# Kernel optimization log

Measured on AMD Instinct MI355X. Metric: run time of the kernel, lower is better.

The kernel has to match this reference:

```python
import jax, jax.numpy as jnp
import numpy as np

# Config (mirrors init_kwargs)
B, S = 1, 2048          # batch, seq_len
H = 2048                # hidden_size
NH, NKV = 16, 8         # attention heads, kv heads (GQA n_rep = 2)
HD = H // NH            # head_dim = 128
I = 5632                # intermediate_size
L = 2                   # num_hidden_layers
V = 32000               # vocab_size
WIN = 1024              # sliding_window
THETA = 10000.0
EPS = 1e-6


def setup_inputs() -> dict:
    key = jax.random.key(0)
    ks = jax.random.split(key, 12)
    s = 0.02
    return {
        "input_ids": jax.random.randint(ks[0], (B, S), 0, V, dtype=jnp.int32),
        "embed": jax.random.normal(ks[1], (V, H), jnp.float32) * s,
        "Wq": jax.random.normal(ks[2], (L, H, NH * HD), jnp.float32) * s,
        "Wk": jax.random.normal(ks[3], (L, H, NKV * HD), jnp.float32) * s,
        "Wv": jax.random.normal(ks[4], (L, H, NKV * HD), jnp.float32) * s,
        "Wo": jax.random.normal(ks[5], (L, NH * HD, H), jnp.float32) * s,
        "Wg": jax.random.normal(ks[6], (L, H, I), jnp.float32) * s,
        "Wu": jax.random.normal(ks[7], (L, H, I), jnp.float32) * s,
        "Wd": jax.random.normal(ks[8], (L, I, H), jnp.float32) * s,
        "ln1": jnp.ones((L, H), jnp.float32),
        "ln2": jnp.ones((L, H), jnp.float32),
        "norm_w": jnp.ones((H,), jnp.float32),
    }


def _rmsnorm(x, w, eps=EPS):
    return x * jax.lax.rsqrt(jnp.mean(x * x, axis=-1, keepdims=True) + eps) * w


def _rope_tables(seq_len, dim, theta):
    inv_freq = 1.0 / (theta ** (jnp.arange(0, dim, 2, dtype=jnp.float32) / dim))
    freqs = jnp.arange(seq_len, dtype=jnp.float32)[:, None] * inv_freq[None, :]  # [S, dim/2]
    emb = jnp.concatenate([freqs, freqs], axis=-1)  # [S, dim]
    return jnp.cos(emb), jnp.sin(emb)


def _rotate_half(x):
    half = x.shape[-1] // 2
    return jnp.concatenate([-x[..., half:], x[..., :half]], axis=-1)


def _sliding_window_causal_mask(seq_len, window, dtype):
    i = jnp.arange(seq_len)[:, None]
    j = jnp.arange(seq_len)[None, :]
    allowed = (j <= i) & (j >= i - window)  # band: causal + sliding window
    return jnp.where(allowed, 0.0, jnp.finfo(dtype).min).astype(dtype)[None, None]  # [1,1,S,S]


def _forward(input_ids, embed, Wq, Wk, Wv, Wo, Wg, Wu, Wd, ln1, ln2, norm_w):
    x = embed[input_ids]  # [B,S,H]
    cos, sin = _rope_tables(S, HD, THETA)          # [S,HD]
    cos = cos[None, :, None, :]                    # [1,S,1,HD]
    sin = sin[None, :, None, :]
    mask = _sliding_window_causal_mask(S, WIN, x.dtype)  # [1,1,S,S]
    scale = 1.0 / jnp.sqrt(jnp.float32(HD)).astype(x.dtype)
    n_rep = NH // NKV

    for l in range(L):
        # --- attention block ---
        h = _rmsnorm(x, ln1[l])
        q = (h @ Wq[l]).reshape(B, S, NH, HD)
        k = (h @ Wk[l]).reshape(B, S, NKV, HD)
        v = (h @ Wv[l]).reshape(B, S, NKV, HD)
        q = q * cos + _rotate_half(q) * sin
        k = k * cos + _rotate_half(k) * sin
        # repeat_kv (GQA)
        k = jnp.broadcast_to(k[:, :, :, None, :], (B, S, NKV, n_rep, HD)).reshape(B, S, NH, HD)
        v = jnp.broadcast_to(v[:, :, :, None, :], (B, S, NKV, n_rep, HD)).reshape(B, S, NH, HD)
        scores = jnp.einsum('bshn,bthn->bhst', q, k) * scale + mask  # [B,NH,S,S]
        attn = jax.nn.softmax(scores.astype(jnp.float32), axis=-1).astype(x.dtype)
        o = jnp.einsum('bhst,bthn->bshn', attn, v).reshape(B, S, NH * HD)
        x = x + o @ Wo[l]
        # --- MLP block (SwiGLU) ---
        h = _rmsnorm(x, ln2[l])
        x = x + (jax.nn.silu(h @ Wg[l]) * (h @ Wu[l])) @ Wd[l]

    return _rmsnorm(x, norm_w)


def reference(input_ids, embed, Wq, Wk, Wv, Wo, Wg, Wu, Wd, ln1, ln2, norm_w):
    return _forward(input_ids, embed, Wq, Wk, Wv, Wo, Wg, Wu, Wd, ln1, ln2, norm_w)
```

## Files before the change

### kernel.cpp

```cpp
#include <hip/hip_runtime.h>
#include <stdint.h>

using bf16x8 = __attribute__((ext_vector_type(8))) __bf16;
using f32x4  = __attribute__((ext_vector_type(4))) float;

#define DEVI __device__ __forceinline__

DEVI unsigned short f2b(float f) {
  unsigned int u = __builtin_bit_cast(unsigned int, f);
  u = (u + 0x7FFFu + ((u >> 16) & 1u)) >> 16;
  return (unsigned short)u;
}
DEVI float b2f(unsigned short h) {
  unsigned int u = ((unsigned int)h) << 16;
  return __builtin_bit_cast(float, u);
}
DEVI f32x4 mfma16(bf16x8 a, bf16x8 b, f32x4 c) {
  return __builtin_amdgcn_mfma_f32_16x16x32_bf16(a, b, c, 0, 0, 0);
}
#define GLD(gp, lp) __builtin_amdgcn_global_load_lds( \
    (__attribute__((address_space(1))) void*)(uintptr_t)(gp), \
    (__attribute__((address_space(3))) void*)(uintptr_t)(lp), 16, 0, 0)

static constexpr int S_LEN = 2048;
static constexpr int HDIM  = 2048;
static constexpr int NH    = 16;
static constexpr int NKV   = 8;
static constexpr int HD    = 128;
static constexpr int IFF   = 5632;
static constexpr int WIN   = 1024;

DEVI void rms_finish(float4 v0, float4 v1, const float* __restrict__ w,
                     void* __restrict__ outp, int s, int t, int outf32) {
  float ss = v0.x*v0.x + v0.y*v0.y + v0.z*v0.z + v0.w*v0.w +
             v1.x*v1.x + v1.y*v1.y + v1.z*v1.z + v1.w*v1.w;
  #pragma unroll
  for (int off = 32; off >= 1; off >>= 1) ss += __shfl_xor(ss, off, 64);
  __shared__ float red[4];
  if ((t & 63) == 0) red[t >> 6] = ss;
  __syncthreads();
  ss = red[0] + red[1] + red[2] + red[3];
  float rr = rsqrtf(ss * (1.0f / 2048.0f) + 1e-6f);
  const float4* w4 = (const float4*)w;
  float4 w0 = w4[t], w1 = w4[t + 256];
  float o0x = v0.x*rr*w0.x, o0y = v0.y*rr*w0.y, o0z = v0.z*rr*w0.z, o0w = v0.w*rr*w0.w;
  float o1x = v1.x*rr*w1.x, o1y = v1.y*rr*w1.y, o1z = v1.z*rr*w1.z, o1w = v1.w*rr*w1.w;
  if (outf32) {
    float4* o4 = (float4*)outp + (size_t)s * 512;
    o4[t]       = make_float4(o0x, o0y, o0z, o0w);
    o4[t + 256] = make_float4(o1x, o1y, o1z, o1w);
  } else {
    uint2* ob = (uint2*)((unsigned short*)outp + (size_t)s * HDIM);
    ob[t]       = make_uint2((unsigned)f2b(o0x) | ((unsigned)f2b(o0y) << 16),
                             (unsigned)f2b(o0z) | ((unsigned)f2b(o0w) << 16));
    ob[t + 256] = make_uint2((unsigned)f2b(o1x) | ((unsigned)f2b(o1y) << 16),
                             (unsigned)f2b(o1z) | ((unsigned)f2b(o1w) << 16));
  }
}

__global__ __launch_bounds__(256) void gather_kernel(const int* __restrict__ ids,
    const float* __restrict__ embed, float* __restrict__ x,
    float* __restrict__ ct, float* __restrict__ st,
    const float* __restrict__ ln1w, unsigned short* __restrict__ h) {
  int s = blockIdx.x, t = threadIdx.x;
  const float4* src = (const float4*)(embed + (size_t)ids[s] * HDIM);
  float4* dst = (float4*)(x + (size_t)s * HDIM);
  float4 v0 = src[t], v1 = src[t + 256];
  dst[t]       = v0;
  dst[t + 256] = v1;
  if (t < 64) {
    float inv = expf(-(float)t * (9.210340371976184f / 64.0f));
    float f = (float)s * inv;
    ct[s * 64 + t] = cosf(f);
    st[s * 64 + t] = sinf(f);
  }
  rms_finish(v0, v1, ln1w, h, s, t, 0);
}

template<int OUTF32, int NPARTS>
__global__ __launch_bounds__(256) void rmsnorm_combine_kernel(
    float* __restrict__ x, const unsigned short* __restrict__ parts,
    const float* __restrict__ w, void* __restrict__ outp) {
  int s = blockIdx.x, t = threadIdx.x;
  const size_t PS = (size_t)2048 * 2048;
  float4* row = (float4*)(x + (size_t)s * HDIM);
  float4 v0 = row[t], v1 = row[t + 256];
  #pragma unroll
  for (int p = 0; p < NPARTS; ++p) {
    const unsigned short* pr = parts + p * PS + (size_t)s * HDIM;
    uint2 a = *(const uint2*)(pr + t * 4);
    uint2 b = *(const uint2*)(pr + (t + 256) * 4);
    v0.x += b2f((unsigned short)a.x); v0.y += b2f((unsigned short)(a.x >> 16));
    v0.z += b2f((unsigned short)a.y); v0.w += b2f((unsigned short)(a.y >> 16));
    v1.x += b2f((unsigned short)b.x); v1.y += b2f((unsigned short)(b.x >> 16));
    v1.z += b2f((unsigned short)b.y); v1.w += b2f((unsigned short)(b.y >> 16));
  }
  row[t] = v0; row[t + 256] = v1;
  rms_finish(v0, v1, w, outp, s, t, OUTF32);
}

__global__ __launch_bounds__(256) void convert_weights_kernel(
    const float* __restrict__ Wq, const float* __restrict__ Wk,
    const float* __restrict__ Wv, const float* __restrict__ Wo,
    const float* __restrict__ Wg, const float* __restrict__ Wu,
    const float* __restrict__ Wd,
    unsigned short* wqkvT, unsigned short* woT,
    unsigned short* wguT, unsigned short* wdT) {
  __shared__ float tl[128 * 65];
  int b = blockIdx.x;
  const float* in; unsigned short* out; int istr, ostr, tilesN, t; int guAdd = -1;
  if (b < 512)       { in = Wq; out = wqkvT;                       istr = 2048; ostr = 2048; tilesN = 32; t = b; }
  else if (b < 768)  { in = Wk; out = wqkvT + (size_t)2048 * 2048; istr = 1024; ostr = 2048; tilesN = 16; t = b - 512; }
  else if (b < 1024) { in = Wv; out = wqkvT + (size_t)3072 * 2048; istr = 1024; ostr = 2048; tilesN = 16; t = b - 768; }
  else if (b < 1536) { in = Wo; out = woT;                         istr = 2048; ostr = 2048; tilesN = 32; t = b - 1024; }
  else if (b < 2944) { in = Wg; out = wguT;                        istr = 5632; ostr = 2048; tilesN = 88; t = b - 1536; guAdd = 0; }
  else if (b < 4352) { in = Wu; out = wguT;                        istr = 5632; ostr = 2048; tilesN = 88; t = b - 2944; guAdd = 128; }
  else               { in = Wd; out = wdT;                         istr = 2048; ostr = 5632; tilesN = 32; t = b - 4352; }
  int k0 = (t / tilesN) * 128, n0 = (t % tilesN) * 64;
  int tx = threadIdx.x & 63, ty = threadIdx.x >> 6;
  #pragma unroll
  for (int i = 0; i < 32; ++i)
    tl[(ty + 4 * i) * 65 + tx] = in[(size_t)(k0 + ty + 4 * i) * istr + (n0 + tx)];
  __syncthreads();
  int ob = (guAdd >= 0) ? (((n0 >> 7) << 8) + (n0 & 64) + guAdd) : n0;
  unsigned int* ou = (unsigned int*)out;
  const int kstr2 = ostr >> 1;
  #pragma unroll
  for (int i = 0; i < 16; ++i) {
    int nrow = ty + 4 * i;
    float lo = tl[(2 * tx) * 65 + nrow], hi = tl[(2 * tx + 1) * 65 + nrow];
    ou[(size_t)(ob + nrow) * kstr2 + (k0 >> 1) + tx] =
        (unsigned int)f2b(lo) | ((unsigned int)f2b(hi) << 16);
  }
}

DEVI bf16x8 ldsAB(const unsigned short* buf, int r, int cbyte) {
  return *(const bf16x8*)((const unsigned char*)buf + r * 128 + (cbyte ^ ((r & 7) << 4)));
}
DEVI void stage_unit(const unsigned short* __restrict__ G, int Kstr,
                     unsigned short* lbuf, int loff0, int grow0,
                     int loff1, int grow1, int w, int l) {
  const int rsub = l >> 3;
  const int ce = ((l & 7) ^ rsub) << 3;
  const unsigned short* s0 = G + (size_t)(grow0 + w * 8 + rsub) * Kstr + ce;
  GLD(s0, (unsigned char*)lbuf + loff0 + w * 1024 + l * 16);
  const unsigned short* s1 = G + (size_t)(grow1 + w * 8 + rsub) * Kstr + ce;
  GLD(s1, (unsigned char*)lbuf + loff1 + w * 1024 + l * 16);
}
template<int Q>
DEVI void phase128(const unsigned short* Ab, f32x4 (&acc)[4][4],
                   bf16x8 (&breg)[2][4], int wr, int lg, int li) {
  const int r0 = wr * 64 + Q * 16 + li;
  bf16x8 a0 = ldsAB(Ab, r0, lg * 16);
  bf16x8 a1 = ldsAB(Ab, r0, 64 + lg * 16);
  __builtin_amdgcn_s_setprio(1);
  #pragma unroll
  for (int n = 0; n < 4; ++n) acc[Q][n] = mfma16(a0, breg[0][n], acc[Q][n]);
  #pragma unroll
  for (int n = 0; n < 4; ++n) acc[Q][n] = mfma16(a1, breg[1][n], acc[Q][n]);
  __builtin_amdgcn_s_setprio(0);
}

template<int EPI>
__global__ __launch_bounds__(512, 1) void gemm128_kernel(
    const unsigned short* __restrict__ A, const unsigned short* __restrict__ Bt,
    void* __restrict__ Cout, int Kstr, int nt, int parts, int nbm, int ldc,
    long long partStride,
    const float* __restrict__ ct, const float* __restrict__ st,
    unsigned short* __restrict__ ko, unsigned short* __restrict__ vt) {
  __shared__ __align__(16) unsigned char smem[131072];
  unsigned short* As0 = (unsigned short*)smem;
  unsigned short* Bs0 = (unsigned short*)(smem + 32768);
  const int tid = threadIdx.x, l = tid & 63, w = tid >> 6;
  const int lg = l >> 4, li = l & 15;
  const int wr = w >> 2, wc = w & 3;
  const int nb = gridDim.x, qx = nb >> 3;
  const int wg = ((int)blockIdx.x & 7) * qx + ((int)blockIdx.x >> 3);
  const int nbT = nb / parts;
  const int tile = wg % nbT, part = wg / nbT;
  const int m0 = (tile % nbm) * 128, n0 = (tile / nbm) * 256;
  const int kOff = part * (nt << 6);
  const unsigned short* At  = A  + (size_t)m0 * Kstr + kOff;
  const unsigned short* Bto = Bt + (size_t)n0 * Kstr + kOff;
  f32x4 acc[4][4] = {};
  bf16x8 breg[2][4];

  stage_unit(Bto, Kstr, Bs0, 0, 0, 8192, 64, w, l);
  stage_unit(Bto, Kstr, Bs0, 16384, 128, 24576, 192, w, l);
  stage_unit(At,  Kstr, As0, 0, 0, 8192, 64, w, l);
  { int k1 = (nt > 1) ? 64 : 0;
    stage_unit(Bto + k1, Kstr, Bs0 + 16384, 0, 0, 8192, 64, w, l);
    stage_unit(Bto + k1, Kstr, Bs0 + 16384, 16384, 128, 24576, 192, w, l); }
  asm volatile("s_waitcnt vmcnt(4)\n\ts_barrier" ::: "memory");

  for (int t = 0; t < nt; ++t) {
    unsigned short* Ab  = As0 + (t & 1) * 8192;
    unsigned short* Bb  = Bs0 + (t & 1) * 16384;
    unsigned short* Abn = As0 + ((t & 1) ^ 1) * 8192;
    const int kt1 = ((t + 1 < nt) ? t + 1 : nt - 1) << 6;
    const int kt2 = ((t + 2 < nt) ? t + 2 : nt - 1) << 6;
    stage_unit(At + kt1, Kstr, Abn, 0, 0, 8192, 64, w, l);
    #pragma unroll
    for (int ks = 0; ks < 2; ++ks)
      #pragma unroll
      for (int n = 0; n < 4; ++n)
        breg[ks][n] = ldsAB(Bb, wc * 64 + n * 16 + li, ks * 64 + lg * 16);
    asm volatile("s_waitcnt lgkmcnt(0)\n\ts_barrier" ::: "memory");
    phase128<0>(Ab, acc, breg, wr, lg, li);
    stage_unit(Bto + kt2, Kstr, Bb, 0, 0, 8192, 64, w, l);
    phase128<1>(Ab, acc, breg, wr, lg, li);
    stage_unit(Bto + kt2, Kstr, Bb, 16384, 128, 24576, 192, w, l);
    phase128<2>(Ab, acc, breg, wr, lg, li);
    phase128<3>(Ab, acc, breg, wr, lg, li);
    asm volatile("s_waitcnt vmcnt(4) lgkmcnt(0)\n\ts_barrier" ::: "memory");
  }
  asm volatile("s_waitcnt vmcnt(0)" ::: "memory");

  if (EPI == 0) {
    unsigned short* C = (unsigned short*)Cout + (size_t)part * (size_t)partStride;
    #pragma unroll
    for (int m = 0; m < 4; ++m)
      #pragma unroll
      for (int n = 0; n < 4; ++n) {
        int col = n0 + wc * 64 + n * 16 + li;
        #pragma unroll
        for (int r = 0; r < 4; ++r) {
          int row = m0 + wr * 64 + m * 16 + lg * 4 + r;
          C[(size_t)row * ldc + col] = f2b(acc[m][n][r]);
        }
      }
  } else if (EPI == 3) {
    float* ub = (float*)smem;
    asm volatile("s_barrier" ::: "memory");
    if (wc >= 2) {
      #pragma unroll
      for (int m = 0; m < 4; ++m)
        #pragma unroll
        for (int n = 0; n < 4; ++n) {
          int colL = (wc - 2) * 64 + n * 16 + li;
          #pragma unroll
          for (int r = 0; r < 4; ++r) {
            int rowl = wr * 64 + m * 16 + lg * 4 + r;
            ub[rowl * 128 + colL] = acc[m][n][r];
          }
        }
    }
    asm volatile("s_waitcnt lgkmcnt(0)\n\ts_barrier" ::: "memory");
    if (wc < 2) {
      unsigned short* act = (unsigned short*)Cout;
      const int col0 = n0 >> 1;
      #pragma unroll
      for (int m = 0; m < 4; ++m)
        #pragma unroll
        for (int n = 0; n < 4; ++n) {
          int colL = wc * 64 + n * 16 + li;
          #pragma unroll
          for (int r = 0; r < 4; ++r) {
            int rowl = wr * 64 + m * 16 + lg * 4 + r;
            float g = acc[m][n][r];
            float u = ub[rowl * 128 + colL];
            act[(size_t)(m0 + rowl) * ldc + col0 + colL] =
                f2b(g / (1.0f + __expf(-g)) * u);
          }
        }
    }
  } else {
    float* dump = (float*)smem;
    asm volatile("s_barrier" ::: "memory");
    #pragma unroll
    for (int m = 0; m < 4; ++m)
      #pragma unroll
      for (int n = 0; n < 4; ++n) {
        int colL = wc * 64 + n * 16 + li;
        #pragma unroll
        for (int r = 0; r < 4; ++r) {
          int rowl = wr * 64 + m * 16 + lg * 4 + r;
          dump[rowl * 256 + colL] = acc[m][n][r];
        }
      }
    asm volatile("s_waitcnt lgkmcnt(0)\n\ts_barrier" ::: "memory");
    if (n0 < 3072) {
      unsigned short* qk = (n0 < 2048) ? (unsigned short*)Cout : ko;
      const int cbase = (n0 < 2048) ? n0 : (n0 - 2048);
      const int ostr  = (n0 < 2048) ? 2048 : 1024;
      #pragma unroll
      for (int m = 0; m < 4; ++m)
        #pragma unroll
        for (int n = 0; n < 4; ++n) {
          int colL = wc * 64 + n * 16 + li;
          int hi = colL & 64;
          #pragma unroll
          for (int r = 0; r < 4; ++r) {
            int rowl = wr * 64 + m * 16 + lg * 4 + r;
            int s = m0 + rowl;
            float own = dump[rowl * 256 + colL];
            float par = dump[rowl * 256 + (colL ^ 64)];
            float c  = ct[s * 64 + (colL & 63)];
            float sn = st[s * 64 + (colL & 63)];
            float v = hi ? (own * c + par * sn) : (own * c - par * sn);
            qk[(size_t)s * ostr + cbase + colL] = f2b(v);
          }
        }
    } else {
      int vcol = tid >> 1, sh = (tid & 1) * 64;
      unsigned short* dstp = vt + (size_t)(n0 - 3072 + vcol) * 2048 + m0 + sh;
      #pragma unroll
      for (int c8 = 0; c8 < 8; ++c8) {
        unsigned short pk[8];
        #pragma unroll
        for (int i = 0; i < 8; ++i)
          pk[i] = f2b(dump[(sh + c8 * 8 + i) * 256 + vcol]);
        *(uint4*)(dstp + c8 * 8) = *(const uint4*)pk;
      }
    }
  }
}

DEVI void stageKV(const unsigned short* __restrict__ kg,
                  const unsigned short* __restrict__ vtg, int kv, int j0,
                  unsigned short* Kbuf, unsigned short* Vbuf, int w, int l) {
  #pragma unroll
  for (int p = 0; p < 2; ++p) {
    int off = p * 8192 + w * 1024 + l * 16;
    int row = off >> 8;
    int colb = (off & 255) ^ ((row & 7) << 4);
    GLD(kg + (size_t)(j0 + row) * (NKV * HD) + kv * HD + (colb >> 1),
        (unsigned char*)Kbuf + off);
  }
  #pragma unroll
  for (int p = 0; p < 2; ++p) {
    int off = p * 8192 + w * 1024 + l * 16;
    int d = off >> 7;
    int colb = (off & 127) ^ ((d & 7) << 4);
    GLD(vtg + (size_t)(kv * HD + d) * S_LEN + j0 + (colb >> 1),
        (unsigned char*)Vbuf + off);
  }
}

__global__ __launch_bounds__(512) void attn_kernel(
    const unsigned short* __restrict__ qg, const unsigned short* __restrict__ kg,
    const unsigned short* __restrict__ vtg, unsigned short* __restrict__ og) {
  __shared__ __align__(16) unsigned short Kl[2][64 * 128];
  __shared__ __align__(16) unsigned short Vtl[2][128 * 64];
  __shared__ __align__(16) unsigned short Plds[8][16 * 72];
  const int tid = threadIdx.x, l = tid & 63, w = tid >> 6;
  const int lg = l >> 4, li = l & 15;
  const int i0 = blockIdx.x * 64, kv = blockIdx.y;
  const int hq = kv * 2 + (w >> 2);
  const int qr0 = i0 + (w & 3) * 16;
  const float scale = 0.08838834764831845f;

  bf16x8 qf[4];
  {
    const unsigned short* qrow = qg + (size_t)(qr0 + li) * (NH * HD) + hq * HD;
    #pragma unroll
    for (int sl = 0; sl < 4; ++sl)
      qf[sl] = *(const bf16x8*)(qrow + sl * 32 + lg * 8);
  }
  f32x4 oacc[8] = {};
  float mrow[4] = {-1e30f, -1e30f, -1e30f, -1e30f};
  float srow[4] = {0.f, 0.f, 0.f, 0.f};

  int jstart = i0 - WIN; if (jstart < 0) jstart = 0;
  stageKV(kg, vtg, kv, jstart, Kl[0], Vtl[0], w, l);

  int it = 0;
  for (int j0 = jstart; j0 <= i0; j0 += 64, ++it) {
    const int cur = it & 1;
    asm volatile("s_waitcnt vmcnt(0) lgkmcnt(0)\n\ts_barrier" ::: "memory");
    if (j0 + 64 <= i0)
      stageKV(kg, vtg, kv, j0 + 64, Kl[cur ^ 1], Vtl[cur ^ 1], w, l);
    const unsigned short* Klds  = Kl[cur];
    const unsigned short* Vtlds = Vtl[cur];

    f32x4 sacc[4] = {};
    #pragma unroll
    for (int nt = 0; nt < 4; ++nt) {
      int kr = nt * 16 + li;
      #pragma unroll
      for (int sl = 0; sl < 4; ++sl) {
        int cb = (sl * 64 + lg * 16) ^ ((kr & 7) << 4);
        bf16x8 kf = *(const bf16x8*)&Klds[(kr * 256 + cb) >> 1];
        sacc[nt] = mfma16(qf[sl], kf, sacc[nt]);
      }
    }

    float pv[4][4];
    #pragma unroll
    for (int r = 0; r < 4; ++r) {
      int qi = qr0 + lg * 4 + r;
      float sval[4];
      float tm = -1e30f;
      #pragma unroll
      for (int nt = 0; nt < 4; ++nt) {
        int j = j0 + nt * 16 + li;
        bool ok = (j <= qi) && (j + WIN >= qi);
        float sv = ok ? sacc[nt][r] * scale : -1e30f;
        sval[nt] = sv;
        tm = fmaxf(tm, sv);
      }
      #pragma unroll
      for (int off2 = 1; off2 < 16; off2 <<= 1)
        tm = fmaxf(tm, __shfl_xor(tm, off2, 64));
      float mnew = fmaxf(mrow[r], tm);
      float resc = __expf(mrow[r] - mnew);
      mrow[r] = mnew;
      float rs = 0.f;
      #pragma unroll
      for (int nt = 0; nt < 4; ++nt) {
        float p = (sval[nt] > -9e29f) ? __expf(sval[nt] - mnew) : 0.f;
        pv[nt][r] = p;
        rs += p;
      }
      #pragma unroll
      for (int off2 = 1; off2 < 16; off2 <<= 1)
        rs += __shfl_xor(rs, off2, 64);
      srow[r] = srow[r] * resc + rs;
      #pragma unroll
      for (int dt = 0; dt < 8; ++dt) oacc[dt][r] *= resc;
    }

    #pragma unroll
    for (int r = 0; r < 4; ++r)
      #pragma unroll
      for (int nt = 0; nt < 4; ++nt)
        Plds[w][(lg * 4 + r) * 72 + nt * 16 + li] = f2b(pv[nt][r]);
    bf16x8 ap[2];
    #pragma unroll
    for (int ks = 0; ks < 2; ++ks)
      ap[ks] = *(const bf16x8*)&Plds[w][li * 72 + ks * 32 + lg * 8];
    #pragma unroll
    for (int dt = 0; dt < 8; ++dt) {
      int d = dt * 16 + li;
      #pragma unroll
      for (int ks = 0; ks < 2; ++ks) {
        int cb = (ks * 64 + lg * 16) ^ ((d & 7) << 4);
        bf16x8 vf = *(const bf16x8*)&Vtlds[(d * 128 + cb) >> 1];
        oacc[dt] = mfma16(ap[ks], vf, oacc[dt]);
      }
    }
  }

  #pragma unroll
  for (int r = 0; r < 4; ++r) {
    float inv = 1.0f / srow[r];
    int qi = qr0 + lg * 4 + r;
    unsigned short* orow = og + (size_t)qi * (NH * HD) + hq * HD;
    #pragma unroll
    for (int dt = 0; dt < 8; ++dt)
      orow[dt * 16 + li] = f2b(oacc[dt][r] * inv);
  }
}

extern "C" void kernel_launch(void* const* d_in, const int* in_sizes, int n_in,
                              void* d_out, int out_size, void* d_ws, size_t ws_size,
                              hipStream_t stream) {
  const int*   ids   = (const int*)d_in[0];
  const float* embed = (const float*)d_in[1];
  const float* Wq    = (const float*)d_in[2];
  const float* Wk    = (const float*)d_in[3];
  const float* Wv    = (const float*)d_in[4];
  const float* Wo    = (const float*)d_in[5];
  const float* Wg    = (const float*)d_in[6];
  const float* Wu    = (const float*)d_in[7];
  const float* Wd    = (const float*)d_in[8];
  const float* ln1   = (const float*)d_in[9];
  const float* ln2   = (const float*)d_in[10];
  const float* normw = (const float*)d_in[11];

  uint8_t* ws = (uint8_t*)d_ws;
  unsigned short* wqkvT = (unsigned short*)(ws + 0);
  unsigned short* woT   = (unsigned short*)(ws + 16777216ull);
  unsigned short* wguT  = (unsigned short*)(ws + 25165824ull);
  unsigned short* wdT   = (unsigned short*)(ws + 71303168ull);
  float*          x     = (float*)(ws + 94371840ull);
  unsigned short* h     = (unsigned short*)(ws + 111149056ull);
  unsigned short* q     = (unsigned short*)(ws + 119537664ull);
  unsigned short* k     = (unsigned short*)(ws + 127926272ull);
  unsigned short* vt    = (unsigned short*)(ws + 132120576ull);
  unsigned short* o     = (unsigned short*)(ws + 136314880ull);
  unsigned short* act   = (unsigned short*)(ws + 119537664ull);
  unsigned short* pbuf  = (unsigned short*)(ws + 144703488ull);
  float*          cost  = (float*)(ws + 213909504ull);
  float*          sint  = (float*)(ws + 214433792ull);
  const long long PSel = 4194304LL;

  gather_kernel<<<2048, 256, 0, stream>>>(ids, embed, x, cost, sint, ln1, h);

  for (int l = 0; l < 2; ++l) {
    convert_weights_kernel<<<5760, 256, 0, stream>>>(
        Wq + (size_t)l * 2048 * 2048, Wk + (size_t)l * 2048 * 1024,
        Wv + (size_t)l * 2048 * 1024, Wo + (size_t)l * 2048 * 2048,
        Wg + (size_t)l * 2048 * 5632, Wu + (size_t)l * 2048 * 5632,
        Wd + (size_t)l * 5632 * 2048,
        wqkvT, woT, wguT, wdT);
    if (l == 1)
      rmsnorm_combine_kernel<0, 2><<<2048, 256, 0, stream>>>(x, pbuf, ln1 + 2048, h);
    gemm128_kernel<4><<<256, 512, 0, stream>>>(h, wqkvT, q, 2048, 32, 1, 16, 2048, 0,
                                               cost, sint, k, vt);
    attn_kernel<<<dim3(32, 8), 512, 0, stream>>>(q, k, vt, o);
    gemm128_kernel<0><<<256, 512, 0, stream>>>(o, woT, pbuf, 2048, 16, 2, 16, 2048, PSel,
                                               nullptr, nullptr, nullptr, nullptr);
    rmsnorm_combine_kernel<0, 2><<<2048, 256, 0, stream>>>(x, pbuf, ln2 + l * 2048, h);
    gemm128_kernel<3><<<704, 512, 0, stream>>>(h, wguT, act, 2048, 32, 1, 16, 5632, 0,
                                               nullptr, nullptr, nullptr, nullptr);
    gemm128_kernel<0><<<256, 512, 0, stream>>>(act, wdT, pbuf, 5632, 44, 2, 16, 2048, PSel,
                                               nullptr, nullptr, nullptr, nullptr);
  }
  rmsnorm_combine_kernel<1, 2><<<2048, 256, 0, stream>>>(x, pbuf, normw, d_out);
  (void)in_sizes; (void)n_in; (void)out_size; (void)ws_size;
}
```

Baseline: 677.2 us.

## Use 256x256 tiled GEMM with 8-phase pipeline for gate/up SwiGLU projection

Replaces the 128x128-tile gate/up GEMM (EPI 3) with a new 256x256-tile kernel. It uses double-buffered A/B LDS slots, an 8-phase load/compute interleave with barriers, and an XCD-aware block remap, while keeping the fused SiLU*up epilogue. Larger tiles halve the global traffic per FLOP and raise MFMA density for the largest GEMM. The cost is 128 fp32 accumulators per lane, high register pressure and a grid of 352 blocks, which may load the CUs unevenly.

```diff
diff --git a/kernel.cpp b/kernel.cpp
--- a/kernel.cpp
+++ b/kernel.cpp
@@ -147,6 +147,11 @@
   const unsigned short* s1 = G + (size_t)(grow1 + w * 8 + rsub) * Kstr + ce;
   GLD(s1, (unsigned char*)lbuf + loff1 + w * 1024 + l * 16);
 }
+DEVI void stage128(const unsigned short* __restrict__ G, int Kstr,
+                   unsigned short* slotbase, int h, int w, int l) {
+  stage_unit(G, Kstr, slotbase, h * 16384, h * 128, h * 16384 + 8192, h * 128 + 64, w, l);
+}
+
 template<int Q>
 DEVI void phase128(const unsigned short* Ab, f32x4 (&acc)[4][4],
                    bf16x8 (&breg)[2][4], int wr, int lg, int li) {
@@ -229,41 +234,6 @@
           C[(size_t)row * ldc + col] = f2b(acc[m][n][r]);
         }
       }
-  } else if (EPI == 3) {
-    float* ub = (float*)smem;
-    asm volatile("s_barrier" ::: "memory");
-    if (wc >= 2) {
-      #pragma unroll
-      for (int m = 0; m < 4; ++m)
-        #pragma unroll
-        for (int n = 0; n < 4; ++n) {
-          int colL = (wc - 2) * 64 + n * 16 + li;
-          #pragma unroll
-          for (int r = 0; r < 4; ++r) {
-            int rowl = wr * 64 + m * 16 + lg * 4 + r;
-            ub[rowl * 128 + colL] = acc[m][n][r];
-          }
-        }
-    }
-    asm volatile("s_waitcnt lgkmcnt(0)\n\ts_barrier" ::: "memory");
-    if (wc < 2) {
-      unsigned short* act = (unsigned short*)Cout;
-      const int col0 = n0 >> 1;
-      #pragma unroll
-      for (int m = 0; m < 4; ++m)
-        #pragma unroll
-        for (int n = 0; n < 4; ++n) {
-          int colL = wc * 64 + n * 16 + li;
-          #pragma unroll
-          for (int r = 0; r < 4; ++r) {
-            int rowl = wr * 64 + m * 16 + lg * 4 + r;
-            float g = acc[m][n][r];
-            float u = ub[rowl * 128 + colL];
-            act[(size_t)(m0 + rowl) * ldc + col0 + colL] =
-                f2b(g / (1.0f + __expf(-g)) * u);
-          }
-        }
-    }
   } else {
     float* dump = (float*)smem;
     asm volatile("s_barrier" ::: "memory");
@@ -316,6 +286,133 @@
   }
 }
 
+template<int Q>
+DEVI void ph256(const unsigned short* Ab, f32x4 (&acc)[8][4],
+                bf16x8 (&breg)[2][4], int wr, int lg, int li) {
+  bf16x8 a[2][2];
+  #pragma unroll
+  for (int mi = 0; mi < 2; ++mi)
+    #pragma unroll
+    for (int ks = 0; ks < 2; ++ks)
+      a[mi][ks] = ldsAB(Ab, wr * 128 + Q * 32 + mi * 16 + li, ks * 64 + lg * 16);
+  asm volatile("s_barrier" ::: "memory");
+  asm volatile("s_waitcnt lgkmcnt(0)" ::: "memory");
+  __builtin_amdgcn_sched_barrier(0);
+  __builtin_amdgcn_s_setprio(1);
+  #pragma unroll
+  for (int mi = 0; mi < 2; ++mi)
+    #pragma unroll
+    for (int ks = 0; ks < 2; ++ks)
+      #pragma unroll
+      for (int n = 0; n < 4; ++n)
+        acc[Q * 2 + mi][n] = mfma16(a[mi][ks], breg[ks][n], acc[Q * 2 + mi][n]);
+  __builtin_amdgcn_s_setprio(0);
+}
+
+__global__ __launch_bounds__(512, 1) void gemm256p8_kernel(
+    const unsigned short* __restrict__ A, const unsigned short* __restrict__ Bt,
+    unsigned short* __restrict__ Cout, int Kstr, int nt, int nbm, int ldc) {
+  __shared__ __align__(16) unsigned char smem[131072];
+  unsigned short* As = (unsigned short*)smem;
+  unsigned short* Bs = (unsigned short*)(smem + 65536);
+  const int tid = threadIdx.x, l = tid & 63, w = tid >> 6;
+  const int lg = l >> 4, li = l & 15;
+  const int wr = w >> 2, wc = w & 3;
+  const int nb = gridDim.x, qx = nb >> 3;
+  const int wg = ((int)blockIdx.x & 7) * qx + ((int)blockIdx.x >> 3);
+  const int m0 = (wg % nbm) * 256, n0 = (wg / nbm) * 256;
+  const unsigned short* At  = A  + (size_t)m0 * Kstr;
+  const unsigned short* Bto = Bt + (size_t)n0 * Kstr;
+  unsigned short* A0 = As,  * A1 = As + 16384;
+  unsigned short* B0 = Bs,  * B1 = Bs + 16384;
+  f32x4 acc[8][4] = {};
+  bf16x8 breg[2][4];
+
+  stage128(At, Kstr, A0, 0, w, l);
+  stage128(At, Kstr, A0, 1, w, l);
+  stage128(Bto, Kstr, B0, 0, w, l);
+  stage128(Bto, Kstr, B0, 1, w, l);
+  stage128(Bto + 64, Kstr, B1, 0, w, l);
+  stage128(Bto + 64, Kstr, B1, 1, w, l);
+  asm volatile("s_waitcnt vmcnt(4)\n\ts_barrier" ::: "memory");
+
+  const int nt2 = nt >> 1;
+  for (int u = 0; u < nt2; ++u) {
+    const int k1 = 2 * u + 1;
+    const int k2 = (2 * u + 2 < nt) ? 2 * u + 2 : nt - 2;
+    const int k3 = (2 * u + 3 < nt) ? 2 * u + 3 : nt - 1;
+    #pragma unroll
+    for (int ks = 0; ks < 2; ++ks)
+      #pragma unroll
+      for (int n = 0; n < 4; ++n)
+        breg[ks][n] = ldsAB(B0, wc * 64 + n * 16 + li, ks * 64 + lg * 16);
+    stage128(At + (k1 << 6), Kstr, A1, 0, w, l);
+    ph256<0>(A0, acc, breg, wr, lg, li);
+    asm volatile("s_barrier" ::: "memory");
+    stage128(At + (k1 << 6), Kstr, A1, 1, w, l);
+    ph256<1>(A0, acc, breg, wr, lg, li);
+    asm volatile("s_barrier" ::: "memory");
+    stage128(Bto + (k2 << 6), Kstr, B0, 0, w, l);
+    ph256<2>(A0, acc, breg, wr, lg, li);
+    asm volatile("s_barrier" ::: "memory");
+    stage128(Bto + (k2 << 6), Kstr, B0, 1, w, l);
+    ph256<3>(A0, acc, breg, wr, lg, li);
+    asm volatile("s_waitcnt vmcnt(4)\n\ts_barrier" ::: "memory");
+    #pragma unroll
+    for (int ks = 0; ks < 2; ++ks)
+      #pragma unroll
+      for (int n = 0; n < 4; ++n)
+        breg[ks][n] = ldsAB(B1, wc * 64 + n * 16 + li, ks * 64 + lg * 16);
+    stage128(At + (k2 << 6), Kstr, A0, 0, w, l);
+    ph256<0>(A1, acc, breg, wr, lg, li);
+    asm volatile("s_barrier" ::: "memory");
+    stage128(At + (k2 << 6), Kstr, A0, 1, w, l);
+    ph256<1>(A1, acc, breg, wr, lg, li);
+    asm volatile("s_barrier" ::: "memory");
+    stage128(Bto + (k3 << 6), Kstr, B1, 0, w, l);
+    ph256<2>(A1, acc, breg, wr, lg, li);
+    asm volatile("s_barrier" ::: "memory");
+    stage128(Bto + (k3 << 6), Kstr, B1, 1, w, l);
+    ph256<3>(A1, acc, breg, wr, lg, li);
+    asm volatile("s_waitcnt vmcnt(4)\n\ts_barrier" ::: "memory");
+  }
+  asm volatile("s_waitcnt vmcnt(0)" ::: "memory");
+
+  float* ub = (float*)smem;
+  asm volatile("s_barrier" ::: "memory");
+  if (wc >= 2) {
+    #pragma unroll
+    for (int m = 0; m < 8; ++m)
+      #pragma unroll
+      for (int n = 0; n < 4; ++n) {
+        int colL = (wc - 2) * 64 + n * 16 + li;
+        #pragma unroll
+        for (int r = 0; r < 4; ++r) {
+          int rowl = wr * 128 + m * 16 + lg * 4 + r;
+          ub[rowl * 128 + colL] = acc[m][n][r];
+        }
+      }
+  }
+  asm volatile("s_waitcnt lgkmcnt(0)\n\ts_barrier" ::: "memory");
+  if (wc < 2) {
+    const int col0 = n0 >> 1;
+    #pragma unroll
+    for (int m = 0; m < 8; ++m)
+      #pragma unroll
+      for (int n = 0; n < 4; ++n) {
+        int colL = wc * 64 + n * 16 + li;
+        #pragma unroll
+        for (int r = 0; r < 4; ++r) {
+          int rowl = wr * 128 + m * 16 + lg * 4 + r;
+          float g = acc[m][n][r];
+          float u = ub[rowl * 128 + colL];
+          Cout[(size_t)(m0 + rowl) * ldc + col0 + colL] =
+              f2b(g / (1.0f + __expf(-g)) * u);
+        }
+      }
+  }
+}
+
 DEVI void stageKV(const unsigned short* __restrict__ kg,
                   const unsigned short* __restrict__ vtg, int kv, int j0,
                   unsigned short* Kbuf, unsigned short* Vbuf, int w, int l) {
@@ -502,8 +599,7 @@
     gemm128_kernel<0><<<256, 512, 0, stream>>>(o, woT, pbuf, 2048, 16, 2, 16, 2048, PSel,
                                                nullptr, nullptr, nullptr, nullptr);
     rmsnorm_combine_kernel<0, 2><<<2048, 256, 0, stream>>>(x, pbuf, ln2 + l * 2048, h);
-    gemm128_kernel<3><<<704, 512, 0, stream>>>(h, wguT, act, 2048, 32, 1, 16, 5632, 0,
-                                               nullptr, nullptr, nullptr, nullptr);
+    gemm256p8_kernel<<<352, 512, 0, stream>>>(h, wguT, act, 2048, 32, 8, 5632);
     gemm128_kernel<0><<<256, 512, 0, stream>>>(act, wdT, pbuf, 5632, 44, 2, 16, 2048, PSel,
                                                nullptr, nullptr, nullptr, nullptr);
   }
```

New measurement: 688.7 us. About the same (+1.7%).
